# Kernel optimization log

Measured on AMD Instinct MI355X. Metric: run time of the kernel, lower is better.

The kernel has to match this reference:

```python
import jax, jax.numpy as jnp
import numpy as np

B, TK, NK, H, E, V = 128, 400, 50, 256, 256, 50000


def setup_inputs() -> dict:
    key = jax.random.key(0)
    ks = iter(jax.random.split(key, 48))
    def rn(shape, s=1.0):
        return jax.random.normal(next(ks), shape, jnp.float32) * s
    def ru(shape):
        return jax.random.uniform(next(ks), shape, jnp.float32)
    z = lambda shape: jnp.zeros(shape, jnp.float32)
    s = 0.05
    inp = {}
    inp['y_t_1'] = jax.random.randint(next(ks), (B,), 0, V)
    inp['h_prev'] = rn((B, H))
    inp['c_prev'] = rn((B, H))
    inp['encoder_outputs'] = rn((B, TK, H))
    inp['encoder_outputs_node'] = rn((B, NK, H))
    inp['enc_padding_mask'] = jnp.ones((B, TK), jnp.float32)
    inp['enc_padding_mask_node'] = jnp.ones((B, NK), jnp.float32)
    inp['c_t_d'] = rn((B, H))
    inp['c_t_g'] = rn((B, H))
    inp['c_t_g2'] = rn((B, H))
    inp['coverage'] = z((B, TK))
    inp['flow'] = ru((B, NK))
    inp['node_to_token'] = ru((B, NK, TK))
    inp['graph'] = ru((B, NK, NK))
    inp['voc_d'] = jax.random.randint(next(ks), (B, TK), 0, V)
    inp['step'] = 0
    # learned parameters
    inp['emb_table'] = rn((V, E), s)
    inp['Wx'] = rn((4 * H, E), s); inp['bx'] = z((E,))
    inp['Wi'] = rn((E, 4 * H), s); inp['Wh'] = rn((H, 4 * H), s)
    inp['bi'] = z((4 * H,)); inp['bh'] = z((4 * H,))
    inp['Whd'] = rn((H, H), s); inp['Wsd'] = rn((2 * H, H), s)
    inp['wcd'] = rn((H,), s); inp['vd'] = rn((H,), s); inp['bd'] = z((H,))
    inp['Wn'] = rn((H, H), s); inp['Wsf'] = rn((2 * H, H), s)
    inp['vf'] = rn((H,), s); inp['bf'] = z((H,))
    inp['Wpg'] = rn((5 * H + E, 1), s); inp['bpg'] = z((1,))
    inp['W1'] = rn((4 * H, H), s); inp['b1'] = z((H,))
    inp['W2'] = rn((H, V), s); inp['b2'] = z((V,))
    return inp


def _forward(y_t_1, h_prev, c_prev, enc, enc_n, mask_t, mask_n, c_t_d, c_t_g, c_t_g2,
             coverage, flow, n2t, graph, voc_d, emb_table, Wx, bx, Wi, Wh, bi, bh,
             Whd, Wsd, wcd, vd, bd, Wn, Wsf, vf, bf, Wpg, bpg, W1, b1, W2, b2):
    sig, tanh = jax.nn.sigmoid, jnp.tanh
    y_emb = emb_table[y_t_1]                                   # [B,E]
    x = jnp.concatenate([c_t_d, c_t_g, c_t_g2, y_emb], 1) @ Wx + bx
    # single-step LSTM (torch gate order i,f,g,o)
    gates = x @ Wi + h_prev @ Wh + bi + bh
    gi, gf, gg, go = jnp.split(gates, 4, axis=1)
    c_new = sig(gf) * c_prev + sig(gi) * tanh(gg)
    h_new = sig(go) * tanh(c_new)
    s_hat = jnp.concatenate([h_new, c_new], 1)                 # [B,2H]
    # doc attention with coverage (Bahdanau)
    e = tanh(enc @ Whd + (s_hat @ Wsd)[:, None, :] + coverage[:, :, None] * wcd + bd) @ vd
    a = jax.nn.softmax(e, axis=1) * mask_t
    a = a / a.sum(1, keepdims=True)                            # [B,TK]
    c_d = jnp.einsum('bt,bth->bh', a, enc)
    coverage_next = coverage + a
    # event-graph node attention (flow-weighted, one-hop propagation)
    en = tanh(enc_n @ Wn + (s_hat @ Wsf)[:, None, :] + bf) @ vf
    an = jax.nn.softmax(en, axis=1) * mask_n
    an = an / an.sum(1, keepdims=True)
    an = an * flow
    an = an / an.sum(1, keepdims=True)                         # [B,NK]
    c_g = jnp.einsum('bn,bnh->bh', an, enc_n)
    an2 = jnp.einsum('bn,bnm->bm', an, graph) * mask_n
    an2 = an2 / an2.sum(1, keepdims=True)
    c_g2 = jnp.einsum('bn,bnh->bh', an2, enc_n)
    a_n2t = jnp.einsum('bn,bnt->bt', an, n2t)
    a_n2t = a_n2t / a_n2t.sum(1, keepdims=True)
    # flow update: per-node max of token attention restricted to node tokens
    flow_ = jnp.max(a[:, None, :] * n2t, axis=2)               # [B,NK]
    flow_next = flow_ / flow_.sum(1, keepdims=True)
    # pointer-generator gate
    p_gen = sig(jnp.concatenate([c_d, c_g, c_g2, s_hat, x], 1) @ Wpg + bpg)  # [B,1]
    out = jnp.concatenate([h_new, c_d, c_g, c_g2], 1) @ W1 + b1
    vocab_dist = jax.nn.softmax(out @ W2 + b2, axis=1)         # [B,V]
    attn_all = a / a.sum(1, keepdims=True)
    attn_ = (1.0 - p_gen) * attn_all
    vocab_ = p_gen * vocab_dist
    rows = jnp.arange(vocab_.shape[0])[:, None]
    final_dist = vocab_.at[rows, voc_d].add(attn_)             # scatter_add over vocab
    return (final_dist, (h_new, c_new), c_d, c_g, c_g2, a, a_n2t, p_gen,
            coverage_next, flow_next)


def reference(y_t_1, h_prev, c_prev, encoder_outputs, encoder_outputs_node,
              enc_padding_mask, enc_padding_mask_node, c_t_d, c_t_g, c_t_g2,
              coverage, flow, node_to_token, graph, voc_d, step,
              emb_table, Wx, bx, Wi, Wh, bi, bh, Whd, Wsd, wcd, vd, bd,
              Wn, Wsf, vf, bf, Wpg, bpg, W1, b1, W2, b2):
    return _forward(y_t_1, h_prev, c_prev, encoder_outputs, encoder_outputs_node,
                    enc_padding_mask, enc_padding_mask_node, c_t_d, c_t_g, c_t_g2,
                    coverage, flow, node_to_token, graph, voc_d, emb_table, Wx, bx,
                    Wi, Wh, bi, bh, Whd, Wsd, wcd, vd, bd, Wn, Wsf, vf, bf,
                    Wpg, bpg, W1, b1, W2, b2)
```

## Files before the change

### kernel.cpp

```cpp
#include <hip/hip_runtime.h>
#include <stdint.h>


typedef unsigned short u16;
typedef unsigned int   u32;

#define Bv  128
#define TKv 400
#define NKv 50
#define Hv  256
#define Vv  50000
#define VPAD 50176
#define NSv 16
#define CHUNKv 3136
#define MDOC (Bv * TKv)
#define MNODE (Bv * NKv)
#define NBLK (VPAD / 64)

typedef __attribute__((ext_vector_type(8))) short bf16x8;
typedef __attribute__((ext_vector_type(4))) float f32x4;

__device__ float g_x[32768];
__device__ float g_xp[4 * 32768];
__device__ float g_gates[131072];
__device__ float g_h[32768];
__device__ float g_c[32768];
__device__ float g_sdp[2 * 32768];
__device__ float g_sfp[2 * 32768];
__device__ float g_ep[4 * MDOC];
__device__ float g_enp[4 * MNODE];
__device__ float g_a[51200];
__device__ float g_cd[32768];
__device__ float g_cdp[8 * 32768];
__device__ float g_cg[32768];
__device__ float g_cg2[32768];
__device__ float g_pg[128];
__device__ float g_ans[MNODE];
__device__ float g_inv4[128];
__device__ float g_fl[MNODE];
__device__ float g_nrs[MNODE];
__device__ float g_o1[32768];
__device__ __attribute__((aligned(16))) u16 g_o1b[32768];
__device__ float g_vpp[(size_t)2 * Bv * NBLK];
__device__ float g_vred[Bv * 2];
__device__ float g_logits[6400000];
__device__ u16   g_Wdt[256 * 256];
__device__ u16   g_Wnt[256 * 256];
__device__ u16   g_W2t[(size_t)VPAD * 256];
__device__ u16   g_encb[(size_t)Bv * TKv * 256];
__device__ u16   g_encnb[(size_t)Bv * NKv * 256];

__device__ __forceinline__ float sigm(float x) { return 1.f / (1.f + expf(-x)); }

__device__ __forceinline__ u16 f2bf(float f) {
    u32 u = __float_as_uint(f);
    return (u16)((u + 0x7fffu + ((u >> 16) & 1u)) >> 16);
}

__device__ __forceinline__ bf16x8 cvt8(const float* __restrict__ p) {
    const float4 a = *(const float4*)p;
    const float4 b = *(const float4*)(p + 4);
    bf16x8 r;
    r[0] = (short)f2bf(a.x); r[1] = (short)f2bf(a.y);
    r[2] = (short)f2bf(a.z); r[3] = (short)f2bf(a.w);
    r[4] = (short)f2bf(b.x); r[5] = (short)f2bf(b.y);
    r[6] = (short)f2bf(b.z); r[7] = (short)f2bf(b.w);
    return r;
}

__device__ __forceinline__ float fast_tanh(float x) {
    x = fminf(fmaxf(x, -15.f), 15.f);
    float e = __expf(2.f * x);
    return (e - 1.f) / (e + 1.f);
}

__device__ __forceinline__ void ms_merge(float& m1, float& s1, float m2, float s2) {
    float M = fmaxf(m1, m2);
    s1 = s1 * expf(m1 - M) + s2 * expf(m2 - M);
    m1 = M;
}

__global__ __launch_bounds__(256) void k_cvt(
    const float* __restrict__ src, u16* __restrict__ dst, int n8)
{
    int i = blockIdx.x * 256 + threadIdx.x;
    const int stride = gridDim.x * 256;
    for (; i < n8; i += stride)
        *(bf16x8*)(dst + (size_t)i * 8) = cvt8(src + (size_t)i * 8);
}

__global__ __launch_bounds__(256) void k_tc(
    const float* __restrict__ src, u16* __restrict__ dst, int K, int N)
{
    __shared__ float tile[32][33];
    const int n0 = blockIdx.x * 32, k0 = blockIdx.y * 32;
    const int tx = threadIdx.x & 31, ty = threadIdx.x >> 5;
    #pragma unroll
    for (int i = 0; i < 32; i += 8) {
        int k = k0 + ty + i, n = n0 + tx;
        tile[ty + i][tx] = (n < N) ? src[(size_t)k * N + n] : 0.f;
    }
    __syncthreads();
    #pragma unroll
    for (int i = 0; i < 32; i += 8) {
        int n = n0 + ty + i, k = k0 + tx;
        dst[(size_t)n * K + k] = f2bf(tile[tx][ty + i]);
    }
}

__global__ __launch_bounds__(256) void k_x(
    const int* __restrict__ y,
    const float* __restrict__ ctd, const float* __restrict__ ctg,
    const float* __restrict__ ctg2, const float* __restrict__ emb,
    const float* __restrict__ Wx)
{
    const int b = blockIdx.x, ks = blockIdx.y, j = threadIdx.x;
    __shared__ float cs[256];
    float v;
    if      (ks == 0) v = ctd [b * 256 + j];
    else if (ks == 1) v = ctg [b * 256 + j];
    else if (ks == 2) v = ctg2[b * 256 + j];
    else              v = emb[(size_t)y[b] * 256 + j];
    cs[j] = v;
    __syncthreads();

    float acc = 0.f;
    const float* w = Wx + (size_t)(ks * 256) * 256 + j;
    #pragma unroll 8
    for (int k = 0; k < 256; k++) acc += cs[k] * w[(size_t)k * 256];
    g_xp[ks * 32768 + b * 256 + j] = acc;
}

__global__ __launch_bounds__(256) void k_gates(
    const float* __restrict__ h_prev,
    const float* __restrict__ Wi, const float* __restrict__ Wh,
    const float* __restrict__ bi, const float* __restrict__ bh,
    const float* __restrict__ bx)
{
    const int b = blockIdx.x, cc = blockIdx.y, j = threadIdx.x;
    __shared__ float xs[256], hs[256];

    float xv = bx[j] + g_xp[b * 256 + j] + g_xp[32768 + b * 256 + j]
             + g_xp[65536 + b * 256 + j] + g_xp[98304 + b * 256 + j];
    xs[j] = xv;
    if (cc == 0) g_x[b * 256 + j] = xv;
    hs[j] = h_prev[b * 256 + j];
    __syncthreads();

    const int col = cc * 256 + j;
    float acc = bi[col] + bh[col];
    const float* wi = Wi + col;
    const float* wh = Wh + col;
    #pragma unroll 8
    for (int k = 0; k < 256; k++)
        acc += xs[k] * wi[(size_t)k * 1024] + hs[k] * wh[(size_t)k * 1024];
    g_gates[b * 1024 + col] = acc;
}

__global__ __launch_bounds__(256) void k_cellsd(
    const float* __restrict__ c_prev,
    const float* __restrict__ Wsd, const float* __restrict__ Wsf,
    float* __restrict__ out_h, float* __restrict__ out_c)
{
    const int b = blockIdx.x, ks = blockIdx.y, j = threadIdx.x;
    __shared__ float sh[256];

    const float* gb = g_gates + b * 1024;
    float gi_ = gb[j], gf_ = gb[256 + j], gg_ = gb[512 + j], go_ = gb[768 + j];
    float cp = c_prev[b * 256 + j];
    float cn = sigm(gf_) * cp + sigm(gi_) * tanhf(gg_);
    float hn = sigm(go_) * tanhf(cn);
    if (ks == 0) {
        g_h[b * 256 + j] = hn;  g_c[b * 256 + j] = cn;
        out_h[b * 256 + j] = hn; out_c[b * 256 + j] = cn;
    }
    sh[j] = (ks == 0) ? hn : cn;
    __syncthreads();

    float asd = 0.f, asf = 0.f;
    const float* wd = Wsd + (size_t)(ks * 256) * 256 + j;
    const float* wf = Wsf + (size_t)(ks * 256) * 256 + j;
    #pragma unroll 8
    for (int k = 0; k < 256; k++) {
        float sv = sh[k];
        asd += sv * wd[(size_t)k * 256];
        asf += sv * wf[(size_t)k * 256];
    }
    g_sdp[ks * 32768 + b * 256 + j] = asd;
    g_sfp[ks * 32768 + b * 256 + j] = asf;
}

template<int R>
__global__ __launch_bounds__(256) void k_scores(
    const u16* __restrict__ srcb,
    const u16* __restrict__ Wt,
    const float* __restrict__ addv0,
    const float* __restrict__ addv1,
    const float* __restrict__ abias,
    const float* __restrict__ cov,
    const float* __restrict__ wcw,
    const float* __restrict__ vv,
    float* __restrict__ eout, int Mtot)
{
    const int tid = threadIdx.x;
    const int lane = tid & 63, w = tid >> 6;
    const int nlow = lane & 15, quad = lane >> 4;
    const int c0 = blockIdx.y * 64;

    __shared__ u16 Bs[64][264];
    {
        const u16* wsrc = Wt + (size_t)c0 * 256;
        #pragma unroll
        for (int j = 0; j < 8; j++) {
            int chunk = tid + j * 256;
            int row = chunk >> 5, c16 = chunk & 31;
            *(bf16x8*)(&Bs[row][c16 * 8]) =
                *(const bf16x8*)(wsrc + row * 256 + c16 * 8);
        }
    }
    __syncthreads();

    const int rowbase = blockIdx.x * 128 + w * 32;
    const u16* a0 = srcb + (size_t)(rowbase + nlow) * 256 + quad * 8;
    const u16* a1 = a0 + 16 * 256;

    const f32x4 zf = {0.f, 0.f, 0.f, 0.f};
    f32x4 acc[2][4];
    #pragma unroll
    for (int mi = 0; mi < 2; mi++)
        #pragma unroll
        for (int ni = 0; ni < 4; ni++) acc[mi][ni] = zf;

    bf16x8 af0 = *(const bf16x8*)(a0);
    bf16x8 af1 = *(const bf16x8*)(a1);
    for (int k0 = 0; k0 < 256; k0 += 32) {
        const int kn = (k0 + 32) & 255;
        bf16x8 nf0 = *(const bf16x8*)(a0 + kn);
        bf16x8 nf1 = *(const bf16x8*)(a1 + kn);
        bf16x8 bf[4];
        #pragma unroll
        for (int ni = 0; ni < 4; ni++)
            bf[ni] = *(const bf16x8*)(&Bs[ni * 16 + nlow][k0 + quad * 8]);
        #pragma unroll
        for (int ni = 0; ni < 4; ni++) {
            acc[0][ni] = __builtin_amdgcn_mfma_f32_16x16x32_bf16(af0, bf[ni], acc[0][ni], 0, 0, 0);
            acc[1][ni] = __builtin_amdgcn_mfma_f32_16x16x32_bf16(af1, bf[ni], acc[1][ni], 0, 0, 0);
        }
        af0 = nf0; af1 = nf1;
    }

    #pragma unroll
    for (int mi = 0; mi < 2; mi++) {
        float covt[4]; int bidx[4];
        #pragma unroll
        for (int r = 0; r < 4; r++) {
            int row = rowbase + mi * 16 + quad * 4 + r;
            covt[r] = cov ? cov[row] : 0.f;
            bidx[r] = row / R;
        }
        float s4[4] = {0.f, 0.f, 0.f, 0.f};
        #pragma unroll
        for (int ni = 0; ni < 4; ni++) {
            int col = c0 + ni * 16 + nlow;
            float vvc = vv[col];
            float ab  = abias[col];
            float wcc = wcw ? wcw[col] : 0.f;
            #pragma unroll
            for (int r = 0; r < 4; r++) {
                float adc = addv0[bidx[r] * 256 + col] + addv1[bidx[r] * 256 + col] + ab;
                s4[r] += vvc * fast_tanh(acc[mi][ni][r] + adc + covt[r] * wcc);
            }
        }
        #pragma unroll
        for (int r = 0; r < 4; r++) {
            float s = s4[r];
            s += __shfl_xor(s, 1, 64);
            s += __shfl_xor(s, 2, 64);
            s += __shfl_xor(s, 4, 64);
            s += __shfl_xor(s, 8, 64);
            int row = rowbase + mi * 16 + quad * 4 + r;
            if (nlow == 0)
                eout[(size_t)blockIdx.y * Mtot + row] = s;
        }
    }
}

__global__ __launch_bounds__(256) void k_doc(
    const float* __restrict__ mask,
    const float* __restrict__ cov,
    float* __restrict__ out_a, float* __restrict__ out_cov)
{
    const int b = blockIdx.x, tid = threadIdx.x;
    __shared__ float red[256];

    float e0 = 0.f, e1s = 0.f;
    #pragma unroll
    for (int ch = 0; ch < 4; ch++) {
        e0 += g_ep[ch * MDOC + b * TKv + tid];
        if (tid + 256 < TKv) e1s += g_ep[ch * MDOC + b * TKv + tid + 256];
    }
    float e1 = (tid + 256 < TKv) ? e1s : -1e30f;

    float m = fmaxf(e0, e1);
    red[tid] = m; __syncthreads();
    for (int s = 128; s > 0; s >>= 1) { if (tid < s) red[tid] = fmaxf(red[tid], red[tid + s]); __syncthreads(); }
    m = red[0]; __syncthreads();

    float p0 = expf(e0 - m) * mask[b * TKv + tid];
    float p1 = (tid + 256 < TKv) ? expf(e1 - m) * mask[b * TKv + tid + 256] : 0.f;
    red[tid] = p0 + p1; __syncthreads();
    for (int s = 128; s > 0; s >>= 1) { if (tid < s) red[tid] += red[tid + s]; __syncthreads(); }
    float inv = 1.f / red[0];

    float a0 = p0 * inv;
    g_a[b * TKv + tid] = a0;
    out_a[b * TKv + tid] = a0;
    out_cov[b * TKv + tid] = cov[b * TKv + tid] + a0;
    if (tid + 256 < TKv) {
        float a1 = p1 * inv;
        g_a[b * TKv + tid + 256] = a1;
        out_a[b * TKv + tid + 256] = a1;
        out_cov[b * TKv + tid + 256] = cov[b * TKv + tid + 256] + a1;
    }
}

__global__ __launch_bounds__(256) void k_cd(const float* __restrict__ enc)
{
    const int b = blockIdx.x, ks = blockIdx.y, tid = threadIdx.x;
    __shared__ float as_[50];
    if (tid < 50) as_[tid] = g_a[b * TKv + ks * 50 + tid];
    __syncthreads();

    const float* eb = enc + ((size_t)b * TKv + ks * 50) * 256 + tid;
    float acc = 0.f;
    #pragma unroll 10
    for (int t = 0; t < 50; t++) acc += as_[t] * eb[(size_t)t * 256];
    g_cdp[ks * 32768 + b * 256 + tid] = acc;
}

__global__ __launch_bounds__(256) void k_fmax(const float* __restrict__ n2t)
{
    const int bn = blockIdx.x;
    const int b = bn / NKv;
    const int tid = threadIdx.x;
    __shared__ float rmx[256], rsm[256];

    const float* nb = n2t + (size_t)bn * TKv;
    const float* ab = g_a + b * TKv;

    float x0 = nb[tid], a0 = ab[tid];
    float mx = a0 * x0, sm = x0;
    if (tid + 256 < TKv) {
        float x1 = nb[tid + 256], a1 = ab[tid + 256];
        mx = fmaxf(mx, a1 * x1);
        sm += x1;
    }
    mx = fmaxf(mx, 0.f);
    rmx[tid] = mx; rsm[tid] = sm; __syncthreads();
    for (int s = 128; s > 0; s >>= 1) {
        if (tid < s) {
            rmx[tid] = fmaxf(rmx[tid], rmx[tid + s]);
            rsm[tid] += rsm[tid + s];
        }
        __syncthreads();
    }
    if (tid == 0) { g_fl[bn] = rmx[0]; g_nrs[bn] = rsm[0]; }
}

__global__ __launch_bounds__(64) void k_flow2(float* __restrict__ out_flow)
{
    const int b = blockIdx.x, tid = threadIdx.x;
    float v = (tid < NKv) ? g_fl[b * NKv + tid] : 0.f;
    float s = v;
    s += __shfl_xor(s, 1, 64);
    s += __shfl_xor(s, 2, 64);
    s += __shfl_xor(s, 4, 64);
    s += __shfl_xor(s, 8, 64);
    s += __shfl_xor(s, 16, 64);
    s += __shfl_xor(s, 32, 64);
    if (tid < NKv) out_flow[b * NKv + tid] = v / s;
}

__global__ __launch_bounds__(256) void k_node1(
    const float* __restrict__ encn,
    const float* __restrict__ maskn,
    const float* __restrict__ flow,
    const float* __restrict__ graph,
    const float* __restrict__ Wpg, const float* __restrict__ bpg,
    float* __restrict__ out_cd, float* __restrict__ out_cg,
    float* __restrict__ out_cg2, float* __restrict__ out_pgen)
{
    const int b = blockIdx.x, tid = threadIdx.x;
    __shared__ float ans[NKv], an2s[NKv], red[256];

    float cd = 0.f;
    #pragma unroll
    for (int i = 0; i < 8; i++) cd += g_cdp[i * 32768 + b * 256 + tid];
    g_cd[b * 256 + tid] = cd;
    out_cd[b * 256 + tid] = cd;

    float v = -1e30f;
    if (tid < NKv) {
        v = 0.f;
        #pragma unroll
        for (int ch = 0; ch < 4; ch++) v += g_enp[ch * MNODE + b * NKv + tid];
    }
    red[tid] = v; __syncthreads();
    for (int s = 128; s > 0; s >>= 1) { if (tid < s) red[tid] = fmaxf(red[tid], red[tid + s]); __syncthreads(); }
    float m = red[0]; __syncthreads();

    float p = (tid < NKv) ? expf(v - m) * maskn[b * NKv + tid] : 0.f;
    red[tid] = p; __syncthreads();
    for (int s = 128; s > 0; s >>= 1) { if (tid < s) red[tid] += red[tid + s]; __syncthreads(); }
    float S = red[0]; __syncthreads();
    p = (tid < NKv) ? (p / S) * flow[b * NKv + tid] : 0.f;
    red[tid] = p; __syncthreads();
    for (int s = 128; s > 0; s >>= 1) { if (tid < s) red[tid] += red[tid + s]; __syncthreads(); }
    float S2 = red[0]; __syncthreads();
    if (tid < NKv) {
        ans[tid] = p / S2;
        g_ans[b * NKv + tid] = ans[tid];
    }
    __syncthreads();

    float s4p = (tid < NKv) ? ans[tid] * g_nrs[b * NKv + tid] : 0.f;
    red[tid] = s4p; __syncthreads();
    for (int s = 128; s > 0; s >>= 1) { if (tid < s) red[tid] += red[tid + s]; __syncthreads(); }
    if (tid == 0) g_inv4[b] = 1.f / red[0];
    __syncthreads();

    float q = 0.f;
    if (tid < NKv) {
        const float* gb = graph + (size_t)b * NKv * NKv + tid;
        #pragma unroll
        for (int n = 0; n < NKv; n++) q += ans[n] * gb[n * NKv];
        q *= maskn[b * NKv + tid];
    }
    red[tid] = q; __syncthreads();
    for (int s = 128; s > 0; s >>= 1) { if (tid < s) red[tid] += red[tid + s]; __syncthreads(); }
    float S3 = red[0]; __syncthreads();
    if (tid < NKv) an2s[tid] = q / S3;
    __syncthreads();

    float cg = 0.f, cg2 = 0.f;
    {
        const float* enb = encn + (size_t)b * NKv * 256 + tid;
        #pragma unroll
        for (int n = 0; n < NKv; n++) {
            float e = enb[n * 256];
            cg  += ans[n]  * e;
            cg2 += an2s[n] * e;
        }
    }
    g_cg[b * 256 + tid] = cg;   out_cg[b * 256 + tid] = cg;
    g_cg2[b * 256 + tid] = cg2; out_cg2[b * 256 + tid] = cg2;

    float hvv = g_h[b * 256 + tid], cvv = g_c[b * 256 + tid];
    float xvv = g_x[b * 256 + tid];
    float part = cd  * Wpg[tid]        + cg  * Wpg[256 + tid]
               + cg2 * Wpg[512 + tid]  + hvv * Wpg[768 + tid]
               + cvv * Wpg[1024 + tid] + xvv * Wpg[1280 + tid];
    red[tid] = part; __syncthreads();
    for (int s = 128; s > 0; s >>= 1) { if (tid < s) red[tid] += red[tid + s]; __syncthreads(); }
    if (tid == 0) {
        float pg = sigm(red[0] + bpg[0]);
        g_pg[b] = pg; out_pgen[b] = pg;
    }
}

__global__ __launch_bounds__(256) void k_ant(
    const float* __restrict__ n2t, float* __restrict__ out_ant)
{
    const int b = blockIdx.x, ks = blockIdx.y, tid = threadIdx.x;
    __shared__ float ans[NKv];
    if (tid < NKv) ans[tid] = g_ans[b * NKv + tid];
    __syncthreads();

    if (tid < 200) {
        const int t = ks * 200 + tid;
        const float* nb = n2t + (size_t)b * NKv * TKv + t;
        float at = 0.f;
        #pragma unroll
        for (int n = 0; n < NKv; n++) at += ans[n] * nb[n * TKv];
        out_ant[b * TKv + t] = at * g_inv4[b];
    }
}

__global__ __launch_bounds__(256) void k_o1(
    const float* __restrict__ W1, const float* __restrict__ b1)
{
    const int b = blockIdx.x, cc = blockIdx.y, tid = threadIdx.x;
    __shared__ float cat[1024];
    __shared__ float red[256];

    cat[tid]       = g_h  [b * 256 + tid];
    cat[256 + tid] = g_cd [b * 256 + tid];
    cat[512 + tid] = g_cg [b * 256 + tid];
    cat[768 + tid] = g_cg2[b * 256 + tid];
    __syncthreads();

    const int lane = tid & 63, kq = tid >> 6;
    const int col = cc * 64 + lane;
    const float* w  = W1 + (size_t)(kq * 256) * 256 + col;
    const float* cs = cat + kq * 256;
    float acc = 0.f;
    #pragma unroll 8
    for (int k = 0; k < 256; k++) acc += cs[k] * w[(size_t)k * 256];
    red[tid] = acc; __syncthreads();

    if (tid < 64) {
        float o = b1[cc * 64 + tid]
                + red[tid] + red[64 + tid] + red[128 + tid] + red[192 + tid];
        g_o1[b * 256 + cc * 64 + tid] = o;
        g_o1b[b * 256 + cc * 64 + tid] = f2bf(o);
    }
}

__global__ __launch_bounds__(256) void k_logits(const float* __restrict__ b2)
{
    const int v0 = blockIdx.x * 64;
    const int tid = threadIdx.x;
    const int lane = tid & 63, wave = tid >> 6;
    const int nlow = lane & 15, quad = lane >> 4;

    const u16* a0p = g_o1b + (wave * 32 + nlow) * 256 + quad * 8;
    const u16* a1p = a0p + 16 * 256;
    const u16* bbase = g_W2t + (size_t)(v0 + nlow) * 256 + quad * 8;

    const f32x4 zf = {0.f, 0.f, 0.f, 0.f};
    f32x4 acc0[4], acc1[4];
    #pragma unroll
    for (int i = 0; i < 4; i++) { acc0[i] = zf; acc1[i] = zf; }

    for (int k0 = 0; k0 < 256; k0 += 32) {
        bf16x8 a0 = *(const bf16x8*)(a0p + k0);
        bf16x8 a1 = *(const bf16x8*)(a1p + k0);
        #pragma unroll
        for (int nt = 0; nt < 4; nt++) {
            bf16x8 bf = *(const bf16x8*)(bbase + (size_t)nt * 4096 + k0);
            acc0[nt] = __builtin_amdgcn_mfma_f32_16x16x32_bf16(a0, bf, acc0[nt], 0, 0, 0);
            acc1[nt] = __builtin_amdgcn_mfma_f32_16x16x32_bf16(a1, bf, acc1[nt], 0, 0, 0);
        }
    }

    float bbv[4]; bool val[4];
    #pragma unroll
    for (int nt = 0; nt < 4; nt++) {
        int v = v0 + nt * 16 + nlow;
        val[nt] = v < Vv;
        bbv[nt] = val[nt] ? b2[v] : 0.f;
    }

    #pragma unroll
    for (int mi = 0; mi < 2; mi++) {
        #pragma unroll
        for (int r = 0; r < 4; r++) {
            const int row = wave * 32 + mi * 16 + quad * 4 + r;
            float x[4];
            #pragma unroll
            for (int nt = 0; nt < 4; nt++) {
                float xv = (mi ? acc1[nt][r] : acc0[nt][r]) + bbv[nt];
                if (val[nt]) g_logits[(size_t)row * Vv + v0 + nt * 16 + nlow] = xv;
                x[nt] = val[nt] ? xv : -1e30f;
            }
            float m = fmaxf(fmaxf(x[0], x[1]), fmaxf(x[2], x[3]));
            m = fmaxf(m, __shfl_xor(m, 1, 64));
            m = fmaxf(m, __shfl_xor(m, 2, 64));
            m = fmaxf(m, __shfl_xor(m, 4, 64));
            m = fmaxf(m, __shfl_xor(m, 8, 64));
            float s = expf(x[0] - m) + expf(x[1] - m)
                    + expf(x[2] - m) + expf(x[3] - m);
            s += __shfl_xor(s, 1, 64);
            s += __shfl_xor(s, 2, 64);
            s += __shfl_xor(s, 4, 64);
            s += __shfl_xor(s, 8, 64);
            if (nlow == 0) {
                g_vpp[((size_t)row * NBLK + blockIdx.x) * 2]     = m;
                g_vpp[((size_t)row * NBLK + blockIdx.x) * 2 + 1] = s;
            }
        }
    }
}

__global__ __launch_bounds__(256) void k_vmerge()
{
    const int b = blockIdx.x, tid = threadIdx.x;
    __shared__ float rm[256], rs[256];

    float M = -1e30f, S = 0.f;
    for (int i = tid; i < NBLK; i += 256)
        ms_merge(M, S, g_vpp[((size_t)b * NBLK + i) * 2],
                       g_vpp[((size_t)b * NBLK + i) * 2 + 1]);
    rm[tid] = M; rs[tid] = S; __syncthreads();
    for (int off = 128; off > 0; off >>= 1) {
        if (tid < off) {
            float m1 = rm[tid], s1 = rs[tid];
            ms_merge(m1, s1, rm[tid + off], rs[tid + off]);
            rm[tid] = m1; rs[tid] = s1;
        }
        __syncthreads();
    }
    if (tid == 0) { g_vred[b * 2] = rm[0]; g_vred[b * 2 + 1] = rs[0]; }
}

__global__ __launch_bounds__(256) void k_vwrite(float* __restrict__ outF)
{
    const int b = blockIdx.x, ks = blockIdx.y, tid = threadIdx.x;

    const float M = g_vred[b * 2];
    const float inv = g_pg[b] / g_vred[b * 2 + 1];

    const int base = ks * CHUNKv;
    const int end  = min(base + CHUNKv, Vv);
    const int n4   = (end - base) >> 2;
    const float4* L4 = (const float4*)(g_logits + (size_t)b * Vv + base);
    float4* O4 = (float4*)(outF + (size_t)b * Vv + base);

    for (int i = tid; i < n4; i += 256) {
        float4 x = L4[i];
        float4 r;
        r.x = expf(x.x - M) * inv;
        r.y = expf(x.y - M) * inv;
        r.z = expf(x.z - M) * inv;
        r.w = expf(x.w - M) * inv;
        O4[i] = r;
    }
}

__global__ __launch_bounds__(256) void k_scatter(
    float* __restrict__ outF, const int* __restrict__ vocd)
{
    const int b = blockIdx.x, tid = threadIdx.x;
    float* Ob = outF + (size_t)b * Vv;
    const float omp = 1.f - g_pg[b];
    for (int t = tid; t < TKv; t += 256)
        atomicAdd(Ob + vocd[b * TKv + t], omp * g_a[b * TKv + t]);
}


extern "C" void kernel_launch(void* const* d_in, const int* in_sizes, int n_in,
                              void* d_out, int out_size, void* d_ws, size_t ws_size,
                              hipStream_t stream)
{
    (void)in_sizes; (void)n_in; (void)out_size; (void)d_ws; (void)ws_size;

    const int*   y      = (const int*)d_in[0];
    const float* h_prev = (const float*)d_in[1];
    const float* c_prev = (const float*)d_in[2];
    const float* enc    = (const float*)d_in[3];
    const float* encn   = (const float*)d_in[4];
    const float* mask   = (const float*)d_in[5];
    const float* maskn  = (const float*)d_in[6];
    const float* ctd    = (const float*)d_in[7];
    const float* ctg    = (const float*)d_in[8];
    const float* ctg2   = (const float*)d_in[9];
    const float* cov    = (const float*)d_in[10];
    const float* flow   = (const float*)d_in[11];
    const float* n2t    = (const float*)d_in[12];
    const float* graph  = (const float*)d_in[13];
    const int*   vocd   = (const int*)d_in[14];
    const float* emb    = (const float*)d_in[16];
    const float* Wx     = (const float*)d_in[17];
    const float* bx     = (const float*)d_in[18];
    const float* Wi     = (const float*)d_in[19];
    const float* Wh     = (const float*)d_in[20];
    const float* bi     = (const float*)d_in[21];
    const float* bh     = (const float*)d_in[22];
    const float* Whd    = (const float*)d_in[23];
    const float* Wsd    = (const float*)d_in[24];
    const float* wcdw   = (const float*)d_in[25];
    const float* vd     = (const float*)d_in[26];
    const float* bd     = (const float*)d_in[27];
    const float* Wn     = (const float*)d_in[28];
    const float* Wsf    = (const float*)d_in[29];
    const float* vf     = (const float*)d_in[30];
    const float* bfv    = (const float*)d_in[31];
    const float* Wpg    = (const float*)d_in[32];
    const float* bpg    = (const float*)d_in[33];
    const float* W1     = (const float*)d_in[34];
    const float* b1     = (const float*)d_in[35];
    const float* W2     = (const float*)d_in[36];
    const float* b2     = (const float*)d_in[37];

    float* o = (float*)d_out;
    float* o_final = o;
    float* o_h     = o + 6400000;
    float* o_c     = o + 6432768;
    float* o_cd    = o + 6465536;
    float* o_cg    = o + 6498304;
    float* o_cg2   = o + 6531072;
    float* o_a     = o + 6563840;
    float* o_ant   = o + 6615040;
    float* o_pg    = o + 6666240;
    float* o_cov   = o + 6666368;
    float* o_fl    = o + 6717568;

    float* g_ep_p;  hipGetSymbolAddress((void**)&g_ep_p,  HIP_SYMBOL(g_ep));
    float* g_enp_p; hipGetSymbolAddress((void**)&g_enp_p, HIP_SYMBOL(g_enp));
    float* g_sdp_p; hipGetSymbolAddress((void**)&g_sdp_p, HIP_SYMBOL(g_sdp));
    float* g_sfp_p; hipGetSymbolAddress((void**)&g_sfp_p, HIP_SYMBOL(g_sfp));
    u16*   g_Wdt_p; hipGetSymbolAddress((void**)&g_Wdt_p, HIP_SYMBOL(g_Wdt));
    u16*   g_Wnt_p; hipGetSymbolAddress((void**)&g_Wnt_p, HIP_SYMBOL(g_Wnt));
    u16*   g_W2t_p; hipGetSymbolAddress((void**)&g_W2t_p, HIP_SYMBOL(g_W2t));
    u16*   g_encb_p;  hipGetSymbolAddress((void**)&g_encb_p,  HIP_SYMBOL(g_encb));
    u16*   g_encnb_p; hipGetSymbolAddress((void**)&g_encnb_p, HIP_SYMBOL(g_encnb));

    k_tc<<<dim3(8, 8), dim3(256), 0, stream>>>(Whd, g_Wdt_p, 256, 256);
    k_tc<<<dim3(8, 8), dim3(256), 0, stream>>>(Wn,  g_Wnt_p, 256, 256);
    k_tc<<<dim3(VPAD / 32, 8), dim3(256), 0, stream>>>(W2, g_W2t_p, 256, Vv);

    k_cvt<<<dim3(2048), dim3(256), 0, stream>>>(enc,  g_encb_p,  Bv * TKv * 256 / 8);
    k_cvt<<<dim3(800),  dim3(256), 0, stream>>>(encn, g_encnb_p, Bv * NKv * 256 / 8);

    k_x<<<dim3(Bv, 4), dim3(256), 0, stream>>>(y, ctd, ctg, ctg2, emb, Wx);

    k_gates<<<dim3(Bv, 4), dim3(256), 0, stream>>>(h_prev, Wi, Wh, bi, bh, bx);

    k_cellsd<<<dim3(Bv, 2), dim3(256), 0, stream>>>(c_prev, Wsd, Wsf, o_h, o_c);

    k_scores<TKv><<<dim3(MDOC / 128, 4), dim3(256), 0, stream>>>(
        g_encb_p, g_Wdt_p, g_sdp_p, g_sdp_p + 32768, bd, cov, wcdw, vd,
        g_ep_p, MDOC);

    k_scores<NKv><<<dim3(MNODE / 128, 4), dim3(256), 0, stream>>>(
        g_encnb_p, g_Wnt_p, g_sfp_p, g_sfp_p + 32768, bfv,
        nullptr, nullptr, vf, g_enp_p, MNODE);

    k_doc<<<dim3(Bv), dim3(256), 0, stream>>>(mask, cov, o_a, o_cov);

    k_fmax<<<dim3(Bv * NKv), dim3(256), 0, stream>>>(n2t);

    k_flow2<<<dim3(Bv), dim3(64), 0, stream>>>(o_fl);

    k_cd<<<dim3(Bv, 8), dim3(256), 0, stream>>>(enc);

    k_node1<<<dim3(Bv), dim3(256), 0, stream>>>(
        encn, maskn, flow, graph, Wpg, bpg,
        o_cd, o_cg, o_cg2, o_pg);

    k_ant<<<dim3(Bv, 2), dim3(256), 0, stream>>>(n2t, o_ant);

    k_o1<<<dim3(Bv, 4), dim3(256), 0, stream>>>(W1, b1);

    k_logits<<<dim3(NBLK), dim3(256), 0, stream>>>(b2);

    k_vmerge<<<dim3(Bv), dim3(256), 0, stream>>>();

    k_vwrite<<<dim3(Bv, NSv), dim3(256), 0, stream>>>(o_final);

    k_scatter<<<dim3(Bv), dim3(256), 0, stream>>>(o_final, vocd);
}
```

Before: 466.8 us.

## Fuse small kernels and compute doc scores over all column chunks per block

Merges the two weight transposes and the two bf16 conversions into single launches, folds flow normalization into k_node1, and folds the vocab max/sum merge into k_vwrite so each of its blocks recomputes the per-row reduction. The doc score kernel now loops over all four 64-column chunks inside one block, keeping A fragments in registers and accumulating the score directly, which removes the 4x partial score buffer and its reduction in k_doc. The aim is fewer launches and less global traffic, at the cost of redundant merge work in k_vwrite (16x per row) and less parallelism in the score kernel.

```diff
diff --git a/kernel.cpp b/kernel.cpp
--- a/kernel.cpp
+++ b/kernel.cpp
@@ -27,7 +27,7 @@
 __device__ float g_c[32768];
 __device__ float g_sdp[2 * 32768];
 __device__ float g_sfp[2 * 32768];
-__device__ float g_ep[4 * MDOC];
+__device__ float g_ep[MDOC];
 __device__ float g_enp[4 * MNODE];
 __device__ float g_a[51200];
 __device__ float g_cd[32768];
@@ -42,7 +42,6 @@
 __device__ float g_o1[32768];
 __device__ __attribute__((aligned(16))) u16 g_o1b[32768];
 __device__ float g_vpp[(size_t)2 * Bv * NBLK];
-__device__ float g_vred[Bv * 2];
 __device__ float g_logits[6400000];
 __device__ u16   g_Wdt[256 * 256];
 __device__ u16   g_Wnt[256 * 256];
@@ -80,13 +79,23 @@
     m1 = M;
 }
 
-__global__ __launch_bounds__(256) void k_cvt(
-    const float* __restrict__ src, u16* __restrict__ dst, int n8)
-{
-    int i = blockIdx.x * 256 + threadIdx.x;
-    const int stride = gridDim.x * 256;
-    for (; i < n8; i += stride)
-        *(bf16x8*)(dst + (size_t)i * 8) = cvt8(src + (size_t)i * 8);
+#define CVT_SPLIT 2048
+__global__ __launch_bounds__(256) void k_cvt2(
+    const float* __restrict__ s0, u16* __restrict__ d0, int n8_0,
+    const float* __restrict__ s1, u16* __restrict__ d1, int n8_1,
+    int nblk1)
+{
+    if (blockIdx.x < CVT_SPLIT) {
+        int i = blockIdx.x * 256 + threadIdx.x;
+        const int stride = CVT_SPLIT * 256;
+        for (; i < n8_0; i += stride)
+            *(bf16x8*)(d0 + (size_t)i * 8) = cvt8(s0 + (size_t)i * 8);
+    } else {
+        int i = (blockIdx.x - CVT_SPLIT) * 256 + threadIdx.x;
+        const int stride = nblk1 * 256;
+        for (; i < n8_1; i += stride)
+            *(bf16x8*)(d1 + (size_t)i * 8) = cvt8(s1 + (size_t)i * 8);
+    }
 }
 
 __global__ __launch_bounds__(256) void k_tc(
@@ -106,6 +115,24 @@
         int n = n0 + ty + i, k = k0 + tx;
         dst[(size_t)n * K + k] = f2bf(tile[tx][ty + i]);
     }
+}
+
+__global__ __launch_bounds__(256) void k_tc_pair(
+    const float* __restrict__ s0, u16* __restrict__ d0,
+    const float* __restrict__ s1, u16* __restrict__ d1)
+{
+    const float* src = blockIdx.z ? s1 : s0;
+    u16* dst = blockIdx.z ? d1 : d0;
+    __shared__ float tile[32][33];
+    const int n0 = blockIdx.x * 32, k0 = blockIdx.y * 32;
+    const int tx = threadIdx.x & 31, ty = threadIdx.x >> 5;
+    #pragma unroll
+    for (int i = 0; i < 32; i += 8)
+        tile[ty + i][tx] = src[(size_t)(k0 + ty + i) * 256 + n0 + tx];
+    __syncthreads();
+    #pragma unroll
+    for (int i = 0; i < 32; i += 8)
+        dst[(size_t)(n0 + ty + i) * 256 + k0 + tx] = f2bf(tile[tx][ty + i]);
 }
 
 __global__ __launch_bounds__(256) void k_x(
@@ -191,7 +218,7 @@
 }
 
 template<int R>
-__global__ __launch_bounds__(256) void k_scores(
+__global__ __launch_bounds__(256) void k_scores_f(
     const u16* __restrict__ srcb,
     const u16* __restrict__ Wt,
     const float* __restrict__ addv0,
@@ -200,6 +227,95 @@
     const float* __restrict__ cov,
     const float* __restrict__ wcw,
     const float* __restrict__ vv,
+    float* __restrict__ eout)
+{
+    const int tid = threadIdx.x;
+    const int lane = tid & 63, w = tid >> 6;
+    const int nlow = lane & 15, quad = lane >> 4;
+
+    __shared__ u16 Bs[64][264];
+
+    const int rowbase = blockIdx.x * 64 + w * 16;
+    const u16* ap = srcb + (size_t)(rowbase + nlow) * 256 + quad * 8;
+
+    bf16x8 areg[8];
+    #pragma unroll
+    for (int kk = 0; kk < 8; kk++)
+        areg[kk] = *(const bf16x8*)(ap + kk * 32);
+
+    float covt[4]; int bidx[4];
+    #pragma unroll
+    for (int r = 0; r < 4; r++) {
+        int row = rowbase + quad * 4 + r;
+        covt[r] = cov ? cov[row] : 0.f;
+        bidx[r] = row / R;
+    }
+
+    float s4[4] = {0.f, 0.f, 0.f, 0.f};
+
+    for (int ch = 0; ch < 4; ch++) {
+        const int c0 = ch * 64;
+        if (ch) __syncthreads();
+        {
+            const u16* wsrc = Wt + (size_t)c0 * 256;
+            #pragma unroll
+            for (int j = 0; j < 8; j++) {
+                int chunk = tid + j * 256;
+                int row = chunk >> 5, c16 = chunk & 31;
+                *(bf16x8*)(&Bs[row][c16 * 8]) =
+                    *(const bf16x8*)(wsrc + row * 256 + c16 * 8);
+            }
+        }
+        __syncthreads();
+
+        const f32x4 zf = {0.f, 0.f, 0.f, 0.f};
+        f32x4 acc[4];
+        #pragma unroll
+        for (int ni = 0; ni < 4; ni++) acc[ni] = zf;
+
+        #pragma unroll
+        for (int kk = 0; kk < 8; kk++) {
+            const int k0 = kk * 32;
+            #pragma unroll
+            for (int ni = 0; ni < 4; ni++) {
+                bf16x8 bf = *(const bf16x8*)(&Bs[ni * 16 + nlow][k0 + quad * 8]);
+                acc[ni] = __builtin_amdgcn_mfma_f32_16x16x32_bf16(
+                    areg[kk], bf, acc[ni], 0, 0, 0);
+            }
+        }
+
+        #pragma unroll
+        for (int ni = 0; ni < 4; ni++) {
+            int col = c0 + ni * 16 + nlow;
+            float vvc = vv[col];
+            float ab  = abias[col];
+            float wcc = wcw ? wcw[col] : 0.f;
+            #pragma unroll
+            for (int r = 0; r < 4; r++) {
+                float adc = addv0[bidx[r] * 256 + col] + addv1[bidx[r] * 256 + col] + ab;
+                s4[r] += vvc * fast_tanh(acc[ni][r] + adc + covt[r] * wcc);
+            }
+        }
+    }
+
+    #pragma unroll
+    for (int r = 0; r < 4; r++) {
+        float s = s4[r];
+        s += __shfl_xor(s, 1, 64);
+        s += __shfl_xor(s, 2, 64);
+        s += __shfl_xor(s, 4, 64);
+        s += __shfl_xor(s, 8, 64);
+        int row = rowbase + quad * 4 + r;
+        if (nlow == 0) eout[row] = s;
+    }
+}
+
+template<int R>
+__global__ __launch_bounds__(256) void k_scores(
+    const u16* __restrict__ srcb, const u16* __restrict__ Wt,
+    const float* __restrict__ addv0, const float* __restrict__ addv1,
+    const float* __restrict__ abias, const float* __restrict__ cov,
+    const float* __restrict__ wcw, const float* __restrict__ vv,
     float* __restrict__ eout, int Mtot)
 {
     const int tid = threadIdx.x;
@@ -293,13 +409,8 @@
     const int b = blockIdx.x, tid = threadIdx.x;
     __shared__ float red[256];
 
-    float e0 = 0.f, e1s = 0.f;
-    #pragma unroll
-    for (int ch = 0; ch < 4; ch++) {
-        e0 += g_ep[ch * MDOC + b * TKv + tid];
-        if (tid + 256 < TKv) e1s += g_ep[ch * MDOC + b * TKv + tid + 256];
-    }
-    float e1 = (tid + 256 < TKv) ? e1s : -1e30f;
+    float e0 = g_ep[b * TKv + tid];
+    float e1 = (tid + 256 < TKv) ? g_ep[b * TKv + tid + 256] : -1e30f;
 
     float m = fmaxf(e0, e1);
     red[tid] = m; __syncthreads();
@@ -367,20 +478,6 @@
     if (tid == 0) { g_fl[bn] = rmx[0]; g_nrs[bn] = rsm[0]; }
 }
 
-__global__ __launch_bounds__(64) void k_flow2(float* __restrict__ out_flow)
-{
-    const int b = blockIdx.x, tid = threadIdx.x;
-    float v = (tid < NKv) ? g_fl[b * NKv + tid] : 0.f;
-    float s = v;
-    s += __shfl_xor(s, 1, 64);
-    s += __shfl_xor(s, 2, 64);
-    s += __shfl_xor(s, 4, 64);
-    s += __shfl_xor(s, 8, 64);
-    s += __shfl_xor(s, 16, 64);
-    s += __shfl_xor(s, 32, 64);
-    if (tid < NKv) out_flow[b * NKv + tid] = v / s;
-}
-
 __global__ __launch_bounds__(256) void k_node1(
     const float* __restrict__ encn,
     const float* __restrict__ maskn,
@@ -388,10 +485,17 @@
     const float* __restrict__ graph,
     const float* __restrict__ Wpg, const float* __restrict__ bpg,
     float* __restrict__ out_cd, float* __restrict__ out_cg,
-    float* __restrict__ out_cg2, float* __restrict__ out_pgen)
+    float* __restrict__ out_cg2, float* __restrict__ out_pgen,
+    float* __restrict__ out_flow)
 {
     const int b = blockIdx.x, tid = threadIdx.x;
     __shared__ float ans[NKv], an2s[NKv], red[256];
+
+    float fv = (tid < NKv) ? g_fl[b * NKv + tid] : 0.f;
+    red[tid] = fv; __syncthreads();
+    for (int s = 128; s > 0; s >>= 1) { if (tid < s) red[tid] += red[tid + s]; __syncthreads(); }
+    float fs = red[0]; __syncthreads();
+    if (tid < NKv) out_flow[b * NKv + tid] = fv / fs;
 
     float cd = 0.f;
     #pragma unroll
@@ -582,9 +686,9 @@
     }
 }
 
-__global__ __launch_bounds__(256) void k_vmerge()
-{
-    const int b = blockIdx.x, tid = threadIdx.x;
+__global__ __launch_bounds__(256) void k_vwrite(float* __restrict__ outF)
+{
+    const int b = blockIdx.x, ks = blockIdx.y, tid = threadIdx.x;
     __shared__ float rm[256], rs[256];
 
     float M = -1e30f, S = 0.f;
@@ -600,15 +704,8 @@
         }
         __syncthreads();
     }
-    if (tid == 0) { g_vred[b * 2] = rm[0]; g_vred[b * 2 + 1] = rs[0]; }
-}
-
-__global__ __launch_bounds__(256) void k_vwrite(float* __restrict__ outF)
-{
-    const int b = blockIdx.x, ks = blockIdx.y, tid = threadIdx.x;
-
-    const float M = g_vred[b * 2];
-    const float inv = g_pg[b] / g_vred[b * 2 + 1];
+    M = rm[0];
+    const float inv = g_pg[b] / rs[0];
 
     const int base = ks * CHUNKv;
     const int end  = min(base + CHUNKv, Vv);
@@ -705,12 +802,12 @@
     u16*   g_encb_p;  hipGetSymbolAddress((void**)&g_encb_p,  HIP_SYMBOL(g_encb));
     u16*   g_encnb_p; hipGetSymbolAddress((void**)&g_encnb_p, HIP_SYMBOL(g_encnb));
 
-    k_tc<<<dim3(8, 8), dim3(256), 0, stream>>>(Whd, g_Wdt_p, 256, 256);
-    k_tc<<<dim3(8, 8), dim3(256), 0, stream>>>(Wn,  g_Wnt_p, 256, 256);
+    k_tc_pair<<<dim3(8, 8, 2), dim3(256), 0, stream>>>(Whd, g_Wdt_p, Wn, g_Wnt_p);
     k_tc<<<dim3(VPAD / 32, 8), dim3(256), 0, stream>>>(W2, g_W2t_p, 256, Vv);
 
-    k_cvt<<<dim3(2048), dim3(256), 0, stream>>>(enc,  g_encb_p,  Bv * TKv * 256 / 8);
-    k_cvt<<<dim3(800),  dim3(256), 0, stream>>>(encn, g_encnb_p, Bv * NKv * 256 / 8);
+    k_cvt2<<<dim3(CVT_SPLIT + 100), dim3(256), 0, stream>>>(
+        enc,  g_encb_p,  Bv * TKv * 256 / 8,
+        encn, g_encnb_p, Bv * NKv * 256 / 8, 100);
 
     k_x<<<dim3(Bv, 4), dim3(256), 0, stream>>>(y, ctd, ctg, ctg2, emb, Wx);
 
@@ -718,9 +815,8 @@
 
     k_cellsd<<<dim3(Bv, 2), dim3(256), 0, stream>>>(c_prev, Wsd, Wsf, o_h, o_c);
 
-    k_scores<TKv><<<dim3(MDOC / 128, 4), dim3(256), 0, stream>>>(
-        g_encb_p, g_Wdt_p, g_sdp_p, g_sdp_p + 32768, bd, cov, wcdw, vd,
-        g_ep_p, MDOC);
+    k_scores_f<TKv><<<dim3(MDOC / 64), dim3(256), 0, stream>>>(
+        g_encb_p, g_Wdt_p, g_sdp_p, g_sdp_p + 32768, bd, cov, wcdw, vd, g_ep_p);
 
     k_scores<NKv><<<dim3(MNODE / 128, 4), dim3(256), 0, stream>>>(
         g_encnb_p, g_Wnt_p, g_sfp_p, g_sfp_p + 32768, bfv,
@@ -730,13 +826,11 @@
 
     k_fmax<<<dim3(Bv * NKv), dim3(256), 0, stream>>>(n2t);
 
-    k_flow2<<<dim3(Bv), dim3(64), 0, stream>>>(o_fl);
-
     k_cd<<<dim3(Bv, 8), dim3(256), 0, stream>>>(enc);
 
     k_node1<<<dim3(Bv), dim3(256), 0, stream>>>(
         encn, maskn, flow, graph, Wpg, bpg,
-        o_cd, o_cg, o_cg2, o_pg);
+        o_cd, o_cg, o_cg2, o_pg, o_fl);
 
     k_ant<<<dim3(Bv, 2), dim3(256), 0, stream>>>(n2t, o_ant);
 
@@ -744,8 +838,6 @@
 
     k_logits<<<dim3(NBLK), dim3(256), 0, stream>>>(b2);
 
-    k_vmerge<<<dim3(Bv), dim3(256), 0, stream>>>();
-
     k_vwrite<<<dim3(Bv, NSv), dim3(256), 0, stream>>>(o_final);
 
     k_scatter<<<dim3(Bv), dim3(256), 0, stream>>>(o_final, vocd);
```

Measured after the change: 471.8 us. Within noise of the previous version (+1.1%).
